# Performance work log

Measured on AMD Instinct MI355X. Metric: run time of the kernel, lower is better.

## Reference

```python
import jax, jax.numpy as jnp
import numpy as np

N_NODES = 16384
HIDDEN = 128
N_SPECIES = 119


def setup_inputs() -> dict:
    key = jax.random.key(0)
    k1, k2, k3, k4 = jax.random.split(key, 4)
    h_prev = jax.random.normal(k1, (N_NODES, HIDDEN), dtype=jnp.float32)
    m_curr = jax.random.normal(k2, (N_NODES, HIDDEN), dtype=jnp.float32)
    # sorted species indices (fast indexed_linear path in the original module)
    atom_types = jnp.sort(jax.random.randint(k3, (N_NODES,), 0, N_SPECIES))
    # per-species weight, init randn / sqrt(hidden_dim) as in the torch module
    weight = jax.random.normal(k4, (N_SPECIES, HIDDEN * HIDDEN), dtype=jnp.float32) / jnp.sqrt(
        jnp.float32(HIDDEN)
    )
    return {"h_prev": h_prev, "m_curr": m_curr, "atom_types": atom_types, "weight": weight}


def reference(h_prev, m_curr, atom_types, weight):
    # h_new[i] = h_prev[i] + W[Z[i]] @ m_curr[i]
    D = h_prev.shape[-1]
    W = weight.reshape(weight.shape[0], D, D)        # (S, D, D)
    Wg = W[atom_types]                               # (N, D, D) indexed gather
    m_transformed = jnp.einsum("nij,nj->ni", Wg, m_curr)
    return h_prev + m_transformed
```

## Files before the change

### kernel.cpp

```cpp
#include <hip/hip_runtime.h>
#include <hip/hip_bf16.h>
#include <stdint.h>

#define HID 128

typedef __attribute__((ext_vector_type(8))) __bf16 bf16x8;
typedef __attribute__((ext_vector_type(4))) float floatx4;

__device__ inline unsigned short f32_to_bf16_rn(float f) {
    union { float f; unsigned int u; } v; v.f = f;
    unsigned int u = v.u;
    unsigned int r = u + 0x7FFFu + ((u >> 16) & 1u);
    return (unsigned short)(r >> 16);
}

__device__ inline bf16x8 load_cvt8(const float* __restrict__ p) {
    float4 v0 = *(const float4*)(p);
    float4 v1 = *(const float4*)(p + 4);
    unsigned short b[8] = {
        f32_to_bf16_rn(v0.x), f32_to_bf16_rn(v0.y), f32_to_bf16_rn(v0.z), f32_to_bf16_rn(v0.w),
        f32_to_bf16_rn(v1.x), f32_to_bf16_rn(v1.y), f32_to_bf16_rn(v1.z), f32_to_bf16_rn(v1.w)
    };
    return *(const bf16x8*)b;
}

__global__ __launch_bounds__(256, 4) void elem_update_kernel(
    const float* __restrict__ h_prev,
    const float* __restrict__ m_curr,
    const int* __restrict__ atom_types,
    const float* __restrict__ weight,
    float* __restrict__ out)
{
    const int tid  = threadIdx.x;
    const int lane = tid & 63;
    const int wave = tid >> 6;
    const int l15  = lane & 15;
    const int quad = lane >> 4;

    const int wg       = blockIdx.x * 4 + wave;
    const int row_tile = wg >> 2;
    const int cq       = wg & 3;
    const int r0       = row_tile * 16;
    const int c0       = cq * 32;

    const int t = atom_types[r0 + l15];

    int s = 0;
    while (s < 16) {
        const int z = __shfl(t, s);
        unsigned long long neq = __ballot(t != z);
        unsigned bits = (unsigned)(neq & 0xFFFFull) & ~((1u << (s + 1)) - 1u);
        const int e = bits ? (int)__builtin_ctz(bits) : 16;

        const float* __restrict__ Wz = weight + (size_t)z * HID * HID;

        floatx4 acc[2];
        #pragma unroll
        for (int nt = 0; nt < 2; ++nt) {
            #pragma unroll
            for (int r = 0; r < 4; ++r) {
                acc[nt][r] = h_prev[(size_t)(r0 + quad * 4 + r) * HID + c0 + nt * 16 + l15];
            }
        }

        #pragma unroll
        for (int kk = 0; kk < 4; ++kk) {
            bf16x8 a = load_cvt8(m_curr + (size_t)(r0 + l15) * HID + kk * 32 + quad * 8);
            #pragma unroll
            for (int nt = 0; nt < 2; ++nt) {
                bf16x8 b = load_cvt8(Wz + (size_t)(c0 + nt * 16 + l15) * HID + kk * 32 + quad * 8);
                acc[nt] = __builtin_amdgcn_mfma_f32_16x16x32_bf16(a, b, acc[nt], 0, 0, 0);
            }
        }

        #pragma unroll
        for (int nt = 0; nt < 2; ++nt) {
            #pragma unroll
            for (int r = 0; r < 4; ++r) {
                int row = quad * 4 + r;
                if (row >= s && row < e) {
                    size_t idx = (size_t)(r0 + row) * HID + c0 + nt * 16 + l15;
                    out[idx] = acc[nt][r];
                }
            }
        }
        s = e;
    }
}

extern "C" void kernel_launch(void* const* d_in, const int* in_sizes, int n_in,
                              void* d_out, int out_size, void* d_ws, size_t ws_size,
                              hipStream_t stream) {
    const float* h_prev     = (const float*)d_in[0];
    const float* m_curr     = (const float*)d_in[1];
    const int*   atom_types = (const int*)d_in[2];
    const float* weight     = (const float*)d_in[3];
    float*       out        = (float*)d_out;

    const int n_nodes = in_sizes[2];
    const int blocks  = n_nodes / 16;
    elem_update_kernel<<<blocks, 256, 0, stream>>>(h_prev, m_curr, atom_types, weight, out);
}
```

Measured before the change: 87.07 us.

## Split work into 16-column wave tiles, raise occupancy, and pack bf16 conversion with perm

Each wave now computes one 16x16 output tile instead of two 16-column tiles. The grid doubles so that eight waves cover a 16-row tile, and launch bounds ask for 8 blocks per CU, which cuts per-wave registers to raise occupancy. The fp32-to-bf16 conversion now packs pairs with a byte-permute instruction rather than building a short array. The cost is that each of the eight waves reloads the m_curr row tile, re-derives the species segmentation, and has fewer independent MFMAs to hide latency.

```diff
diff --git a/kernel.cpp b/kernel.cpp
--- a/kernel.cpp
+++ b/kernel.cpp
@@ -7,24 +7,26 @@
 typedef __attribute__((ext_vector_type(8))) __bf16 bf16x8;
 typedef __attribute__((ext_vector_type(4))) float floatx4;
 
-__device__ inline unsigned short f32_to_bf16_rn(float f) {
-    union { float f; unsigned int u; } v; v.f = f;
-    unsigned int u = v.u;
-    unsigned int r = u + 0x7FFFu + ((u >> 16) & 1u);
-    return (unsigned short)(r >> 16);
+__device__ inline unsigned int pack2_bf16_rn(float lo, float hi) {
+    unsigned int ulo = __float_as_uint(lo);
+    unsigned int uhi = __float_as_uint(hi);
+    unsigned int rlo = ulo + 0x7FFFu + ((ulo >> 16) & 1u);
+    unsigned int rhi = uhi + 0x7FFFu + ((uhi >> 16) & 1u);
+    return __builtin_amdgcn_perm(rhi, rlo, 0x07060302);
 }
 
 __device__ inline bf16x8 load_cvt8(const float* __restrict__ p) {
     float4 v0 = *(const float4*)(p);
     float4 v1 = *(const float4*)(p + 4);
-    unsigned short b[8] = {
-        f32_to_bf16_rn(v0.x), f32_to_bf16_rn(v0.y), f32_to_bf16_rn(v0.z), f32_to_bf16_rn(v0.w),
-        f32_to_bf16_rn(v1.x), f32_to_bf16_rn(v1.y), f32_to_bf16_rn(v1.z), f32_to_bf16_rn(v1.w)
-    };
-    return *(const bf16x8*)b;
+    uint4 u;
+    u.x = pack2_bf16_rn(v0.x, v0.y);
+    u.y = pack2_bf16_rn(v0.z, v0.w);
+    u.z = pack2_bf16_rn(v1.x, v1.y);
+    u.w = pack2_bf16_rn(v1.z, v1.w);
+    return __builtin_bit_cast(bf16x8, u);
 }
 
-__global__ __launch_bounds__(256, 4) void elem_update_kernel(
+__global__ __launch_bounds__(256, 8) void elem_update_kernel(
     const float* __restrict__ h_prev,
     const float* __restrict__ m_curr,
     const int* __restrict__ atom_types,
@@ -38,10 +40,10 @@
     const int quad = lane >> 4;
 
     const int wg       = blockIdx.x * 4 + wave;
-    const int row_tile = wg >> 2;
-    const int cq       = wg & 3;
+    const int row_tile = wg >> 3;
+    const int co       = wg & 7;
     const int r0       = row_tile * 16;
-    const int c0       = cq * 32;
+    const int c0       = co * 16;
 
     const int t = atom_types[r0 + l15];
 
@@ -54,34 +56,25 @@
 
         const float* __restrict__ Wz = weight + (size_t)z * HID * HID;
 
-        floatx4 acc[2];
+        floatx4 acc;
         #pragma unroll
-        for (int nt = 0; nt < 2; ++nt) {
-            #pragma unroll
-            for (int r = 0; r < 4; ++r) {
-                acc[nt][r] = h_prev[(size_t)(r0 + quad * 4 + r) * HID + c0 + nt * 16 + l15];
-            }
+        for (int r = 0; r < 4; ++r) {
+            acc[r] = h_prev[(size_t)(r0 + quad * 4 + r) * HID + c0 + l15];
         }
 
         #pragma unroll
         for (int kk = 0; kk < 4; ++kk) {
             bf16x8 a = load_cvt8(m_curr + (size_t)(r0 + l15) * HID + kk * 32 + quad * 8);
-            #pragma unroll
-            for (int nt = 0; nt < 2; ++nt) {
-                bf16x8 b = load_cvt8(Wz + (size_t)(c0 + nt * 16 + l15) * HID + kk * 32 + quad * 8);
-                acc[nt] = __builtin_amdgcn_mfma_f32_16x16x32_bf16(a, b, acc[nt], 0, 0, 0);
-            }
+            bf16x8 b = load_cvt8(Wz + (size_t)(c0 + l15) * HID + kk * 32 + quad * 8);
+            acc = __builtin_amdgcn_mfma_f32_16x16x32_bf16(a, b, acc, 0, 0, 0);
         }
 
         #pragma unroll
-        for (int nt = 0; nt < 2; ++nt) {
-            #pragma unroll
-            for (int r = 0; r < 4; ++r) {
-                int row = quad * 4 + r;
-                if (row >= s && row < e) {
-                    size_t idx = (size_t)(r0 + row) * HID + c0 + nt * 16 + l15;
-                    out[idx] = acc[nt][r];
-                }
+        for (int r = 0; r < 4; ++r) {
+            int row = quad * 4 + r;
+            if (row >= s && row < e) {
+                size_t idx = (size_t)(r0 + row) * HID + c0 + l15;
+                out[idx] = acc[r];
             }
         }
         s = e;
@@ -98,6 +91,6 @@
     float*       out        = (float*)d_out;
 
     const int n_nodes = in_sizes[2];
-    const int blocks  = n_nodes / 16;
+    const int blocks  = (n_nodes / 16) * 8 / 4;
     elem_update_kernel<<<blocks, 256, 0, stream>>>(h_prev, m_curr, atom_types, weight, out);
 }
```

Result: slower. 90.04 us (+3.4%).
